# Optimization experiments

Hardware: AMD Instinct MI355X
Metric: run time of the kernel (lower is better)

## Reference

```python
import jax, jax.numpy as jnp
import numpy as np


def setup_inputs() -> dict:
    key = jax.random.key(0)
    ks = jax.random.split(key, 6)
    N, H, W, focal = 1024, 128, 128, 100
    means = jax.random.normal(ks[0], (N, 3), dtype=jnp.float32) * 2.0
    scales = jax.random.uniform(ks[1], (N, 3), dtype=jnp.float32, minval=0.05, maxval=0.2)
    rotations = (jax.random.normal(ks[2], (N, 4), dtype=jnp.float32) * 0.1).at[:, 0].add(1.0)
    colors = jax.random.uniform(ks[3], (N, 3), dtype=jnp.float32)
    opacities = jax.random.normal(ks[4], (N, 1), dtype=jnp.float32) * 0.5
    # camera: identity rotation, translated so Gaussians sit in front (depth ~ 8 +/- 2)
    camera_pose = jnp.eye(4, dtype=jnp.float32).at[2, 3].set(8.0)
    return {"camera_pose": camera_pose, "means": means, "scales": scales,
            "rotations": rotations, "colors": colors, "opacities": opacities,
            "H": H, "W": W, "focal": focal}


def reference(camera_pose, means, scales, rotations, colors, opacities, H, W, focal):
    N = means.shape[0]
    f = jnp.asarray(focal, jnp.float32)
    Rc = camera_pose[:3, :3]
    tc = camera_pose[:3, 3]
    mc = means @ Rc.T + tc                      # [N,3] camera-frame means
    depths = mc[:, 2]
    valid = depths > 0
    Z = jnp.maximum(depths, 1e-10)
    cx = f * mc[:, 0] / Z + W / 2.0
    cy = f * mc[:, 1] / Z + H / 2.0
    # quaternion -> rotation matrix
    q = rotations / jnp.linalg.norm(rotations, axis=1, keepdims=True)
    qw, qx, qy, qz = q[:, 0], q[:, 1], q[:, 2], q[:, 3]
    Rg = jnp.stack([
        1 - 2 * (qy**2 + qz**2), 2 * (qx * qy - qw * qz), 2 * (qx * qz + qw * qy),
        2 * (qx * qy + qw * qz), 1 - 2 * (qx**2 + qz**2), 2 * (qy * qz - qw * qx),
        2 * (qx * qz - qw * qy), 2 * (qy * qz + qw * qx), 1 - 2 * (qx**2 + qy**2)],
        axis=1).reshape(N, 3, 3)
    cov3d = jnp.einsum('nij,nj,nkj->nik', Rg, scales**2, Rg)      # R diag(s^2) R^T
    cov_cam = jnp.einsum('ij,njk,lk->nil', Rc, cov3d, Rc)
    zero = jnp.zeros_like(Z)
    J = jnp.stack([f / Z, zero, -f * mc[:, 0] / (Z * Z),
                   zero, f / Z, -f * mc[:, 1] / (Z * Z)], axis=1).reshape(N, 2, 3)
    cov2d = jnp.einsum('nij,njk,nlk->nil', J, cov_cam, J) + 1e-6 * jnp.eye(2, dtype=jnp.float32)
    a, b, c, d = cov2d[:, 0, 0], cov2d[:, 0, 1], cov2d[:, 1, 0], cov2d[:, 1, 1]
    det = a * d - b * c
    iA, iB, iC, iD = d / det, -b / det, -c / det, a / det        # analytic 2x2 inverse
    radius = 3.0 * jnp.max(jnp.sqrt(jnp.stack([a, d], axis=1) + 1e-10), axis=1)
    culled = (cx < -W / 2.0) | (cx > W * 1.5) | (cy < -H / 2.0) | (cy > H * 1.5)
    # integer bbox with trunc() matching Python int() on the torch side
    x0 = jnp.maximum(0.0, jnp.trunc(cx - radius))
    x1 = jnp.minimum(float(W), jnp.trunc(cx + radius + 1.0))
    y0 = jnp.maximum(0.0, jnp.trunc(cy - radius))
    y1 = jnp.minimum(float(H), jnp.trunc(cy + radius + 1.0))
    active = (valid & ~culled).astype(jnp.float32)
    opac = jax.nn.sigmoid(opacities[:, 0])
    order = jnp.argsort(-depths)                                  # back-to-front
    xs = (cx[order], cy[order], iA[order], iB[order], iC[order], iD[order],
          x0[order], x1[order], y0[order], y1[order],
          opac[order], colors[order], active[order])
    X = jnp.arange(W, dtype=jnp.float32)[None, :]
    Y = jnp.arange(H, dtype=jnp.float32)[:, None]

    def step(carry, g):
        alpha, img = carry
        gcx, gcy, ga, gb, gc, gd, bx0, bx1, by0, by1, op, col, act = g
        dx = X - gcx
        dy = Y - gcy
        wgt = jnp.exp(-0.5 * (ga * dx * dx + (gb + gc) * dx * dy + gd * dy * dy)) * op
        inbox = (X >= bx0) & (X < bx1) & (Y >= by0) & (Y < by1)
        wgt = (wgt * inbox * act)[:, :, None]                     # [H,W,1]
        cur = 1.0 - alpha
        alpha = alpha + wgt * cur
        img = img + col[None, None, :] * (wgt * cur)
        return (alpha, img), None

    init = (jnp.zeros((H, W, 1), jnp.float32), jnp.zeros((H, W, 3), jnp.float32))
    (alpha, img), _ = jax.lax.scan(step, init, xs)
    bg = jnp.zeros(3, jnp.float32)
    return img + bg[None, None, :] * (1.0 - alpha)
```

## Files before the change

### kernel.cpp

```cpp
#include <hip/hip_runtime.h>
#include <math.h>


#define TS   8
#define CAP  1024
#define RTH  512

__device__ __forceinline__ float frcp(float x) { return __builtin_amdgcn_rcpf(x); }

__global__ __launch_bounds__(64) void gs_prep(
    const float* __restrict__ cam,
    const float* __restrict__ means,
    const float* __restrict__ scales,
    const float* __restrict__ rots,
    const float* __restrict__ colors,
    const float* __restrict__ opacs,
    const int* __restrict__ pF,
    unsigned int* __restrict__ pbox,
    float4* __restrict__ qA,
    float4* __restrict__ qB,
    float2* __restrict__ qC,
    float Wf, float Hf, int N)
{
    const int j = blockIdx.x * 64 + threadIdx.x;
    if (j >= N) return;

    const float4 q4 = ((const float4*)rots)[j];
    const float m0 = means[3*j+0], m1 = means[3*j+1], m2 = means[3*j+2];
    const float s0 = scales[3*j+0], s1 = scales[3*j+1], s2 = scales[3*j+2];
    const float cR = colors[3*j+0], cG = colors[3*j+1], cB = colors[3*j+2];
    const float opraw = opacs[j];
    const float f = (float)(*pF);

    const float R00=cam[0], R01=cam[1], R02=cam[2],  t0=cam[3];
    const float R10=cam[4], R11=cam[5], R12=cam[6],  t1=cam[7];
    const float R20=cam[8], R21=cam[9], R22=cam[10], t2=cam[11];

    const float mc0 = R00*m0 + R01*m1 + R02*m2 + t0;
    const float mc1 = R10*m0 + R11*m1 + R12*m2 + t1;
    const float mc2 = R20*m0 + R21*m1 + R22*m2 + t2;
    const float depth = mc2;
    const bool valid = depth > 0.0f;
    const float Z  = fmaxf(depth, 1e-10f);
    const float rZ = frcp(Z);
    const float cx = f * mc0 * rZ + Wf * 0.5f;
    const float cy = f * mc1 * rZ + Hf * 0.5f;

    float qw = q4.x, qx = q4.y, qy = q4.z, qz = q4.w;
    const float rqn = __builtin_amdgcn_rsqf(qw*qw + qx*qx + qy*qy + qz*qz);
    qw *= rqn; qx *= rqn; qy *= rqn; qz *= rqn;
    const float Rg00 = 1.f - 2.f*(qy*qy + qz*qz);
    const float Rg01 = 2.f*(qx*qy - qw*qz);
    const float Rg02 = 2.f*(qx*qz + qw*qy);
    const float Rg10 = 2.f*(qx*qy + qw*qz);
    const float Rg11 = 1.f - 2.f*(qx*qx + qz*qz);
    const float Rg12 = 2.f*(qy*qz - qw*qx);
    const float Rg20 = 2.f*(qx*qz - qw*qy);
    const float Rg21 = 2.f*(qy*qz + qw*qx);
    const float Rg22 = 1.f - 2.f*(qx*qx + qy*qy);

    const float S0 = s0*s0, S1 = s1*s1, S2 = s2*s2;

    const float c300 = Rg00*S0*Rg00 + Rg01*S1*Rg01 + Rg02*S2*Rg02;
    const float c301 = Rg00*S0*Rg10 + Rg01*S1*Rg11 + Rg02*S2*Rg12;
    const float c302 = Rg00*S0*Rg20 + Rg01*S1*Rg21 + Rg02*S2*Rg22;
    const float c311 = Rg10*S0*Rg10 + Rg11*S1*Rg11 + Rg12*S2*Rg12;
    const float c312 = Rg10*S0*Rg20 + Rg11*S1*Rg21 + Rg12*S2*Rg22;
    const float c322 = Rg20*S0*Rg20 + Rg21*S1*Rg21 + Rg22*S2*Rg22;

    const float M00 = R00*c300 + R01*c301 + R02*c302;
    const float M01 = R00*c301 + R01*c311 + R02*c312;
    const float M02 = R00*c302 + R01*c312 + R02*c322;
    const float M10 = R10*c300 + R11*c301 + R12*c302;
    const float M11 = R10*c301 + R11*c311 + R12*c312;
    const float M12 = R10*c302 + R11*c312 + R12*c322;
    const float M20 = R20*c300 + R21*c301 + R22*c302;
    const float M21 = R20*c301 + R21*c311 + R22*c312;
    const float M22 = R20*c302 + R21*c312 + R22*c322;

    const float cc00 = M00*R00 + M01*R01 + M02*R02;
    const float cc01 = M00*R10 + M01*R11 + M02*R12;
    const float cc02 = M00*R20 + M01*R21 + M02*R22;
    const float cc10 = M10*R00 + M11*R01 + M12*R02;
    const float cc11 = M10*R10 + M11*R11 + M12*R12;
    const float cc12 = M10*R20 + M11*R21 + M12*R22;
    const float cc20 = M20*R00 + M21*R01 + M22*R02;
    const float cc21 = M20*R10 + M21*R11 + M22*R12;
    const float cc22 = M20*R20 + M21*R21 + M22*R22;

    const float J00 = f * rZ;
    const float J02 = -f * mc0 * rZ * rZ;
    const float J11 = J00;
    const float J12 = -f * mc1 * rZ * rZ;

    const float T00 = J00*cc00 + J02*cc20;
    const float T01 = J00*cc01 + J02*cc21;
    const float T02 = J00*cc02 + J02*cc22;
    const float T10 = J11*cc10 + J12*cc20;
    const float T11 = J11*cc11 + J12*cc21;
    const float T12 = J11*cc12 + J12*cc22;

    const float a  = T00*J00 + T02*J02 + 1e-6f;
    const float b  = T01*J11 + T02*J12;
    const float c_ = T10*J00 + T12*J02;
    const float d  = T11*J11 + T12*J12 + 1e-6f;

    const float radius = 3.0f * fmaxf(sqrtf(a + 1e-10f), sqrtf(d + 1e-10f));
    const bool culled = (cx < -Wf*0.5f) || (cx > Wf*1.5f) ||
                        (cy < -Hf*0.5f) || (cy > Hf*1.5f);

    unsigned int pk = 0x000000FFu;
    if (valid && !culled) {
        const int x0 = (int)fmaxf(0.0f, truncf(cx - radius));
        const int x1 = (int)fminf(Wf,  truncf(cx + radius + 1.0f));
        const int y0 = (int)fmaxf(0.0f, truncf(cy - radius));
        const int y1 = (int)fminf(Hf,  truncf(cy + radius + 1.0f));
        pk = (unsigned)x0 | ((unsigned)x1 << 8) |
             ((unsigned)y0 << 16) | ((unsigned)y1 << 24);
        const float rdet = frcp(a*d - b*c_);
        const float iA  =  d * rdet;
        const float iBC = (-b * rdet) + (-c_ * rdet);
        const float iD  =  a * rdet;
        const float op  = frcp(1.0f + __expf(-opraw));
        qA[j] = make_float4(cx, cy, iA, iBC);
        qB[j] = make_float4(iD, op, cR, cG);
        qC[j] = make_float2(cB, depth);
    }
    pbox[j] = pk;
}

__global__ __launch_bounds__(RTH) void gs_raster(
    const unsigned int* __restrict__ pbox,
    const float4* __restrict__ qA,
    const float4* __restrict__ qB,
    const float2* __restrict__ qC,
    float* __restrict__ out, int W, int N)
{
    __shared__ unsigned int s_box[CAP];
    __shared__ float4 s_A[CAP];
    __shared__ float4 s_B[CAP];
    __shared__ float2 s_C[CAP];
    __shared__ short  s_j[CAP];
    __shared__ short  s_ord[CAP];
    __shared__ float4 s_seg[8][64];
    __shared__ int    s_cnt;

    const int tid = threadIdx.x;
    if (tid == 0) s_cnt = 0;
    __syncthreads();

    const int tx0 = blockIdx.x * TS, ty0 = blockIdx.y * TS;

    const int nit = (N + RTH - 1) / RTH;
    for (int it = 0; it < nit; ++it) {
        const int j = it * RTH + tid;
        if (j < N) {
            const unsigned int pk = pbox[j];
            const int x0 = pk & 255, x1 = (pk >> 8) & 255;
            const int y0 = (pk >> 16) & 255, y1 = pk >> 24;
            if (x0 < tx0 + TS && x1 > tx0 && y0 < ty0 + TS && y1 > ty0) {
                const int slot = atomicAdd(&s_cnt, 1);
                if (slot < CAP) {
                    s_box[slot] = pk;
                    s_A[slot] = qA[j];
                    s_B[slot] = qB[j];
                    s_C[slot] = qC[j];
                    s_j[slot] = (short)j;
                }
            }
        }
    }
    __syncthreads();
    const int M = (s_cnt < CAP) ? s_cnt : CAP;

    for (int s = tid; s < M; s += RTH) {
        const float ds = s_C[s].y;
        const int   is = s_j[s];
        int rank = 0;
        for (int k = 0; k < M; ++k) {
            const float dk = s_C[k].y;
            const int   ik = s_j[k];
            rank += ((dk > ds) || (dk == ds && ik < is)) ? 1 : 0;
        }
        s_ord[rank] = (short)s;
    }
    __syncthreads();

    const int seg  = tid >> 6;
    const int lane = tid & 63;
    const int xi = tx0 + (lane & (TS - 1));
    const int yi = ty0 + (lane >> 3);
    const float px = (float)xi, py = (float)yi;

    const int Mq = (M + 7) >> 3;
    const int k0 = seg * Mq;
    const int k1 = (k0 + Mq < M) ? (k0 + Mq) : M;

    float T = 1.f, R = 0.f, G = 0.f, B = 0.f;
    for (int k = k0; k < k1; ++k) {
        const int p = s_ord[k];
        const unsigned int pk = s_box[p];
        const int bx0 = pk & 255, bx1 = (pk >> 8) & 255;
        const int by0 = (pk >> 16) & 255, by1 = pk >> 24;
        if (xi >= bx0 && xi < bx1 && yi >= by0 && yi < by1) {
            const float4 a = s_A[p];
            const float4 b = s_B[p];
            const float cb = s_C[p].x;
            const float dx = px - a.x;
            const float dy = py - a.y;
            const float e = -0.5f * (a.z*dx*dx + a.w*dx*dy + b.x*dy*dy);
            const float w = __expf(e) * b.y;
            const float wc = w * T;
            T -= wc;
            R += b.z * wc;
            G += b.w * wc;
            B += cb * wc;
        }
    }
    s_seg[seg][lane] = make_float4(T, R, G, B);
    __syncthreads();

    if (tid < 64) {
        float Tt = 1.f, Rr = 0.f, Gg = 0.f, Bb = 0.f;
        #pragma unroll
        for (int s = 0; s < 8; ++s) {
            const float4 v = s_seg[s][tid];
            Rr += Tt * v.y;
            Gg += Tt * v.z;
            Bb += Tt * v.w;
            Tt *= v.x;
        }
        const int o = (yi * W + xi) * 3;
        out[o+0] = Rr;
        out[o+1] = Gg;
        out[o+2] = Bb;
    }
}

extern "C" void kernel_launch(void* const* d_in, const int* in_sizes, int n_in,
                              void* d_out, int out_size, void* d_ws, size_t ws_size,
                              hipStream_t stream)
{
    const float* cam    = (const float*)d_in[0];
    const float* means  = (const float*)d_in[1];
    const float* scales = (const float*)d_in[2];
    const float* rots   = (const float*)d_in[3];
    const float* colors = (const float*)d_in[4];
    const float* opacs  = (const float*)d_in[5];
    const int*   pF     = (const int*)d_in[8];
    float* out = (float*)d_out;

    const int N = in_sizes[1] / 3;

    const int HW = out_size / 3;
    const int dim = (int)(sqrt((double)HW) + 0.5);

    char* ws = (char*)d_ws;
    unsigned int* pbox = (unsigned int*)ws;
    float4*       qA   = (float4*)(ws + 16384);
    float4*       qB   = (float4*)(ws + 16384 + 16384);
    float2*       qC   = (float2*)(ws + 16384 + 32768);

    gs_prep<<<(N + 63) / 64, 64, 0, stream>>>(cam, means, scales, rots,
                                              colors, opacs, pF,
                                              pbox, qA, qB, qC,
                                              (float)dim, (float)dim, N);

    dim3 grid((dim + TS - 1) / TS, (dim + TS - 1) / TS);
    gs_raster<<<grid, RTH, 0, stream>>>(pbox, qA, qB, qC, out, dim, N);
}
```

Baseline: 78.87 us.

## Fuse Gaussian preprocessing into raster kernel with wave-aggregated compaction

Removes the separate preprocessing kernel. Each raster tile block now recomputes projection, 2D covariance and bounds for every Gaussian itself, then appends the ones that overlap the tile to shared memory. Slots are reserved with one atomic per wavefront using ballot and popcount, instead of one atomic per thread. This drops a kernel launch and the global round trip through workspace buffers, at the cost of repeating the preprocessing work in every block. The chunk loop is capped at two 512-thread passes, so Gaussians beyond 1024 are ignored, which matches the existing shared-memory capacity.

Measured after the change: 77.89 us. About the same (-1.2%).

```diff
diff --git a/kernel.cpp b/kernel.cpp
--- a/kernel.cpp
+++ b/kernel.cpp
@@ -8,7 +8,7 @@
 
 __device__ __forceinline__ float frcp(float x) { return __builtin_amdgcn_rcpf(x); }
 
-__global__ __launch_bounds__(64) void gs_prep(
+__global__ __launch_bounds__(RTH) void gs_fused(
     const float* __restrict__ cam,
     const float* __restrict__ means,
     const float* __restrict__ scales,
@@ -16,125 +16,8 @@
     const float* __restrict__ colors,
     const float* __restrict__ opacs,
     const int* __restrict__ pF,
-    unsigned int* __restrict__ pbox,
-    float4* __restrict__ qA,
-    float4* __restrict__ qB,
-    float2* __restrict__ qC,
-    float Wf, float Hf, int N)
-{
-    const int j = blockIdx.x * 64 + threadIdx.x;
-    if (j >= N) return;
-
-    const float4 q4 = ((const float4*)rots)[j];
-    const float m0 = means[3*j+0], m1 = means[3*j+1], m2 = means[3*j+2];
-    const float s0 = scales[3*j+0], s1 = scales[3*j+1], s2 = scales[3*j+2];
-    const float cR = colors[3*j+0], cG = colors[3*j+1], cB = colors[3*j+2];
-    const float opraw = opacs[j];
-    const float f = (float)(*pF);
-
-    const float R00=cam[0], R01=cam[1], R02=cam[2],  t0=cam[3];
-    const float R10=cam[4], R11=cam[5], R12=cam[6],  t1=cam[7];
-    const float R20=cam[8], R21=cam[9], R22=cam[10], t2=cam[11];
-
-    const float mc0 = R00*m0 + R01*m1 + R02*m2 + t0;
-    const float mc1 = R10*m0 + R11*m1 + R12*m2 + t1;
-    const float mc2 = R20*m0 + R21*m1 + R22*m2 + t2;
-    const float depth = mc2;
-    const bool valid = depth > 0.0f;
-    const float Z  = fmaxf(depth, 1e-10f);
-    const float rZ = frcp(Z);
-    const float cx = f * mc0 * rZ + Wf * 0.5f;
-    const float cy = f * mc1 * rZ + Hf * 0.5f;
-
-    float qw = q4.x, qx = q4.y, qy = q4.z, qz = q4.w;
-    const float rqn = __builtin_amdgcn_rsqf(qw*qw + qx*qx + qy*qy + qz*qz);
-    qw *= rqn; qx *= rqn; qy *= rqn; qz *= rqn;
-    const float Rg00 = 1.f - 2.f*(qy*qy + qz*qz);
-    const float Rg01 = 2.f*(qx*qy - qw*qz);
-    const float Rg02 = 2.f*(qx*qz + qw*qy);
-    const float Rg10 = 2.f*(qx*qy + qw*qz);
-    const float Rg11 = 1.f - 2.f*(qx*qx + qz*qz);
-    const float Rg12 = 2.f*(qy*qz - qw*qx);
-    const float Rg20 = 2.f*(qx*qz - qw*qy);
-    const float Rg21 = 2.f*(qy*qz + qw*qx);
-    const float Rg22 = 1.f - 2.f*(qx*qx + qy*qy);
-
-    const float S0 = s0*s0, S1 = s1*s1, S2 = s2*s2;
-
-    const float c300 = Rg00*S0*Rg00 + Rg01*S1*Rg01 + Rg02*S2*Rg02;
-    const float c301 = Rg00*S0*Rg10 + Rg01*S1*Rg11 + Rg02*S2*Rg12;
-    const float c302 = Rg00*S0*Rg20 + Rg01*S1*Rg21 + Rg02*S2*Rg22;
-    const float c311 = Rg10*S0*Rg10 + Rg11*S1*Rg11 + Rg12*S2*Rg12;
-    const float c312 = Rg10*S0*Rg20 + Rg11*S1*Rg21 + Rg12*S2*Rg22;
-    const float c322 = Rg20*S0*Rg20 + Rg21*S1*Rg21 + Rg22*S2*Rg22;
-
-    const float M00 = R00*c300 + R01*c301 + R02*c302;
-    const float M01 = R00*c301 + R01*c311 + R02*c312;
-    const float M02 = R00*c302 + R01*c312 + R02*c322;
-    const float M10 = R10*c300 + R11*c301 + R12*c302;
-    const float M11 = R10*c301 + R11*c311 + R12*c312;
-    const float M12 = R10*c302 + R11*c312 + R12*c322;
-    const float M20 = R20*c300 + R21*c301 + R22*c302;
-    const float M21 = R20*c301 + R21*c311 + R22*c312;
-    const float M22 = R20*c302 + R21*c312 + R22*c322;
-
-    const float cc00 = M00*R00 + M01*R01 + M02*R02;
-    const float cc01 = M00*R10 + M01*R11 + M02*R12;
-    const float cc02 = M00*R20 + M01*R21 + M02*R22;
-    const float cc10 = M10*R00 + M11*R01 + M12*R02;
-    const float cc11 = M10*R10 + M11*R11 + M12*R12;
-    const float cc12 = M10*R20 + M11*R21 + M12*R22;
-    const float cc20 = M20*R00 + M21*R01 + M22*R02;
-    const float cc21 = M20*R10 + M21*R11 + M22*R12;
-    const float cc22 = M20*R20 + M21*R21 + M22*R22;
-
-    const float J00 = f * rZ;
-    const float J02 = -f * mc0 * rZ * rZ;
-    const float J11 = J00;
-    const float J12 = -f * mc1 * rZ * rZ;
-
-    const float T00 = J00*cc00 + J02*cc20;
-    const float T01 = J00*cc01 + J02*cc21;
-    const float T02 = J00*cc02 + J02*cc22;
-    const float T10 = J11*cc10 + J12*cc20;
-    const float T11 = J11*cc11 + J12*cc21;
-    const float T12 = J11*cc12 + J12*cc22;
-
-    const float a  = T00*J00 + T02*J02 + 1e-6f;
-    const float b  = T01*J11 + T02*J12;
-    const float c_ = T10*J00 + T12*J02;
-    const float d  = T11*J11 + T12*J12 + 1e-6f;
-
-    const float radius = 3.0f * fmaxf(sqrtf(a + 1e-10f), sqrtf(d + 1e-10f));
-    const bool culled = (cx < -Wf*0.5f) || (cx > Wf*1.5f) ||
-                        (cy < -Hf*0.5f) || (cy > Hf*1.5f);
-
-    unsigned int pk = 0x000000FFu;
-    if (valid && !culled) {
-        const int x0 = (int)fmaxf(0.0f, truncf(cx - radius));
-        const int x1 = (int)fminf(Wf,  truncf(cx + radius + 1.0f));
-        const int y0 = (int)fmaxf(0.0f, truncf(cy - radius));
-        const int y1 = (int)fminf(Hf,  truncf(cy + radius + 1.0f));
-        pk = (unsigned)x0 | ((unsigned)x1 << 8) |
-             ((unsigned)y0 << 16) | ((unsigned)y1 << 24);
-        const float rdet = frcp(a*d - b*c_);
-        const float iA  =  d * rdet;
-        const float iBC = (-b * rdet) + (-c_ * rdet);
-        const float iD  =  a * rdet;
-        const float op  = frcp(1.0f + __expf(-opraw));
-        qA[j] = make_float4(cx, cy, iA, iBC);
-        qB[j] = make_float4(iD, op, cR, cG);
-        qC[j] = make_float2(cB, depth);
-    }
-    pbox[j] = pk;
-}
-
-__global__ __launch_bounds__(RTH) void gs_raster(
-    const unsigned int* __restrict__ pbox,
-    const float4* __restrict__ qA,
-    const float4* __restrict__ qB,
-    const float2* __restrict__ qC,
-    float* __restrict__ out, int W, int N)
+    float* __restrict__ out,
+    float Wf, float Hf, int W, int N)
 {
     __shared__ unsigned int s_box[CAP];
     __shared__ float4 s_A[CAP];
@@ -145,27 +28,138 @@
     __shared__ float4 s_seg[8][64];
     __shared__ int    s_cnt;
 
-    const int tid = threadIdx.x;
+    const int tid  = threadIdx.x;
+    const int lane = tid & 63;
     if (tid == 0) s_cnt = 0;
     __syncthreads();
 
     const int tx0 = blockIdx.x * TS, ty0 = blockIdx.y * TS;
-
-    const int nit = (N + RTH - 1) / RTH;
-    for (int it = 0; it < nit; ++it) {
-        const int j = it * RTH + tid;
+    const float ftx0 = (float)tx0, ftx1 = (float)(tx0 + TS);
+    const float fty0 = (float)ty0, fty1 = (float)(ty0 + TS);
+
+    const float R00=cam[0], R01=cam[1], R02=cam[2],  t0=cam[3];
+    const float R10=cam[4], R11=cam[5], R12=cam[6],  t1=cam[7];
+    const float R20=cam[8], R21=cam[9], R22=cam[10], t2=cam[11];
+    const float f = (float)(*pF);
+
+    const int nc = (N + RTH - 1) / RTH;
+    #pragma unroll
+    for (int c = 0; c < 2; ++c) {
+        if (c >= nc) break;
+        const int j = c * RTH + tid;
+        bool hit = false;
+        unsigned int pk = 0;
+        float cx=0.f, cy=0.f, iA=0.f, iBC=0.f, iD=0.f;
+        float op=0.f, cR=0.f, cG=0.f, cB=0.f, depth=0.f;
         if (j < N) {
-            const unsigned int pk = pbox[j];
-            const int x0 = pk & 255, x1 = (pk >> 8) & 255;
-            const int y0 = (pk >> 16) & 255, y1 = pk >> 24;
-            if (x0 < tx0 + TS && x1 > tx0 && y0 < ty0 + TS && y1 > ty0) {
-                const int slot = atomicAdd(&s_cnt, 1);
-                if (slot < CAP) {
-                    s_box[slot] = pk;
-                    s_A[slot] = qA[j];
-                    s_B[slot] = qB[j];
-                    s_C[slot] = qC[j];
-                    s_j[slot] = (short)j;
+            const float4 q4 = ((const float4*)rots)[j];
+            const float m0 = means[3*j+0], m1 = means[3*j+1], m2 = means[3*j+2];
+            const float s0 = scales[3*j+0], s1 = scales[3*j+1], s2 = scales[3*j+2];
+            cR = colors[3*j+0]; cG = colors[3*j+1]; cB = colors[3*j+2];
+            const float opraw = opacs[j];
+
+            const float mc0 = R00*m0 + R01*m1 + R02*m2 + t0;
+            const float mc1 = R10*m0 + R11*m1 + R12*m2 + t1;
+            const float mc2 = R20*m0 + R21*m1 + R22*m2 + t2;
+            depth = mc2;
+            const bool valid = depth > 0.0f;
+            const float Z  = fmaxf(depth, 1e-10f);
+            const float rZ = frcp(Z);
+            cx = f * mc0 * rZ + Wf * 0.5f;
+            cy = f * mc1 * rZ + Hf * 0.5f;
+
+            float qw = q4.x, qx = q4.y, qy = q4.z, qz = q4.w;
+            const float rqn = __builtin_amdgcn_rsqf(qw*qw + qx*qx + qy*qy + qz*qz);
+            qw *= rqn; qx *= rqn; qy *= rqn; qz *= rqn;
+            const float Rg00 = 1.f - 2.f*(qy*qy + qz*qz);
+            const float Rg01 = 2.f*(qx*qy - qw*qz);
+            const float Rg02 = 2.f*(qx*qz + qw*qy);
+            const float Rg10 = 2.f*(qx*qy + qw*qz);
+            const float Rg11 = 1.f - 2.f*(qx*qx + qz*qz);
+            const float Rg12 = 2.f*(qy*qz - qw*qx);
+            const float Rg20 = 2.f*(qx*qz - qw*qy);
+            const float Rg21 = 2.f*(qy*qz + qw*qx);
+            const float Rg22 = 1.f - 2.f*(qx*qx + qy*qy);
+
+            const float S0 = s0*s0, S1 = s1*s1, S2 = s2*s2;
+            const float c300 = Rg00*S0*Rg00 + Rg01*S1*Rg01 + Rg02*S2*Rg02;
+            const float c301 = Rg00*S0*Rg10 + Rg01*S1*Rg11 + Rg02*S2*Rg12;
+            const float c302 = Rg00*S0*Rg20 + Rg01*S1*Rg21 + Rg02*S2*Rg22;
+            const float c311 = Rg10*S0*Rg10 + Rg11*S1*Rg11 + Rg12*S2*Rg12;
+            const float c312 = Rg10*S0*Rg20 + Rg11*S1*Rg21 + Rg12*S2*Rg22;
+            const float c322 = Rg20*S0*Rg20 + Rg21*S1*Rg21 + Rg22*S2*Rg22;
+
+            const float M00 = R00*c300 + R01*c301 + R02*c302;
+            const float M01 = R00*c301 + R01*c311 + R02*c312;
+            const float M02 = R00*c302 + R01*c312 + R02*c322;
+            const float M10 = R10*c300 + R11*c301 + R12*c302;
+            const float M11 = R10*c301 + R11*c311 + R12*c312;
+            const float M12 = R10*c302 + R11*c312 + R12*c322;
+            const float M20 = R20*c300 + R21*c301 + R22*c302;
+            const float M21 = R20*c301 + R21*c311 + R22*c312;
+            const float M22 = R20*c302 + R21*c312 + R22*c322;
+
+            const float cc00 = M00*R00 + M01*R01 + M02*R02;
+            const float cc01 = M00*R10 + M01*R11 + M02*R12;
+            const float cc02 = M00*R20 + M01*R21 + M02*R22;
+            const float cc10 = M10*R00 + M11*R01 + M12*R02;
+            const float cc11 = M10*R10 + M11*R11 + M12*R12;
+            const float cc12 = M10*R20 + M11*R21 + M12*R22;
+            const float cc20 = M20*R00 + M21*R01 + M22*R02;
+            const float cc21 = M20*R10 + M21*R11 + M22*R12;
+            const float cc22 = M20*R20 + M21*R21 + M22*R22;
+
+            const float J00 = f * rZ;
+            const float J02 = -f * mc0 * rZ * rZ;
+            const float J11 = J00;
+            const float J12 = -f * mc1 * rZ * rZ;
+
+            const float T00 = J00*cc00 + J02*cc20;
+            const float T01 = J00*cc01 + J02*cc21;
+            const float T02 = J00*cc02 + J02*cc22;
+            const float T10 = J11*cc10 + J12*cc20;
+            const float T11 = J11*cc11 + J12*cc21;
+            const float T12 = J11*cc12 + J12*cc22;
+
+            const float a  = T00*J00 + T02*J02 + 1e-6f;
+            const float b  = T01*J11 + T02*J12;
+            const float c_ = T10*J00 + T12*J02;
+            const float d  = T11*J11 + T12*J12 + 1e-6f;
+
+            const float radius = 3.0f * fmaxf(sqrtf(a + 1e-10f), sqrtf(d + 1e-10f));
+            const bool culled = (cx < -Wf*0.5f) || (cx > Wf*1.5f) ||
+                                (cy < -Hf*0.5f) || (cy > Hf*1.5f);
+            if (valid && !culled) {
+                const float x0 = fmaxf(0.0f, truncf(cx - radius));
+                const float x1 = fminf(Wf,  truncf(cx + radius + 1.0f));
+                const float y0 = fmaxf(0.0f, truncf(cy - radius));
+                const float y1 = fminf(Hf,  truncf(cy + radius + 1.0f));
+                hit = (x0 < ftx1) && (x1 > ftx0) && (y0 < fty1) && (y1 > fty0);
+                if (hit) {
+                    pk = (unsigned)(int)x0 | ((unsigned)(int)x1 << 8) |
+                         ((unsigned)(int)y0 << 16) | ((unsigned)(int)y1 << 24);
+                    const float rdet = frcp(a*d - b*c_);
+                    iA  =  d * rdet;
+                    iBC = (-b * rdet) + (-c_ * rdet);
+                    iD  =  a * rdet;
+                    op  = frcp(1.0f + __expf(-opraw));
+                }
+            }
+        }
+        const unsigned long long m = __ballot(hit);
+        const int nh = (int)__popcll(m);
+        int base = 0;
+        if (nh) {
+            if (lane == 0 && hit == hit) base = atomicAdd(&s_cnt, nh);
+            base = __shfl(base, 0);
+            if (hit) {
+                const int pos = base + (int)__popcll(m & ((1ull << lane) - 1ull));
+                if (pos < CAP) {
+                    s_box[pos] = pk;
+                    s_A[pos] = make_float4(cx, cy, iA, iBC);
+                    s_B[pos] = make_float4(iD, op, cR, cG);
+                    s_C[pos] = make_float2(cB, depth);
+                    s_j[pos] = (short)j;
                 }
             }
         }
@@ -186,8 +180,7 @@
     }
     __syncthreads();
 
-    const int seg  = tid >> 6;
-    const int lane = tid & 63;
+    const int seg = tid >> 6;
     const int xi = tx0 + (lane & (TS - 1));
     const int yi = ty0 + (lane >> 3);
     const float px = (float)xi, py = (float)yi;
@@ -220,7 +213,7 @@
     s_seg[seg][lane] = make_float4(T, R, G, B);
     __syncthreads();
 
-    if (tid < 64) {
+    if (tid < 64 && xi < W && yi < W) {
         float Tt = 1.f, Rr = 0.f, Gg = 0.f, Bb = 0.f;
         #pragma unroll
         for (int s = 0; s < 8; ++s) {
@@ -255,17 +248,7 @@
     const int HW = out_size / 3;
     const int dim = (int)(sqrt((double)HW) + 0.5);
 
-    char* ws = (char*)d_ws;
-    unsigned int* pbox = (unsigned int*)ws;
-    float4*       qA   = (float4*)(ws + 16384);
-    float4*       qB   = (float4*)(ws + 16384 + 16384);
-    float2*       qC   = (float2*)(ws + 16384 + 32768);
-
-    gs_prep<<<(N + 63) / 64, 64, 0, stream>>>(cam, means, scales, rots,
-                                              colors, opacs, pF,
-                                              pbox, qA, qB, qC,
-                                              (float)dim, (float)dim, N);
-
     dim3 grid((dim + TS - 1) / TS, (dim + TS - 1) / TS);
-    gs_raster<<<grid, RTH, 0, stream>>>(pbox, qA, qB, qC, out, dim, N);
+    gs_fused<<<grid, RTH, 0, stream>>>(cam, means, scales, rots, colors, opacs,
+                                       pF, out, (float)dim, (float)dim, dim, N);
 }
```
